# Performance work log

Hardware: AMD Instinct MI355X
Metric: run time of the kernel (lower is better)

Reference implementation:

```python
import jax, jax.numpy as jnp
import numpy as np

N, P, VEC, M = 100000, 96, 4, 70000
GROUPS = [27, 8, 8]
K = sum(GROUPS)  # 43
# Replicates the original's use of the LOCAL per-group offset index i_k when
# selecting attention weights in the output accumulation loop.
ATTN_IDX = np.concatenate([np.arange(g) for g in GROUPS]).astype(np.int32)


def setup_inputs() -> dict:
    key = jax.random.key(0)
    ks = jax.random.split(key, 12)
    rng = np.random.default_rng(0)
    # Kernel maps: per offset, M (in_idx, out_idx) pairs; out indices unique per
    # offset (each output point has at most one neighbor at a given offset).
    kmaps = np.stack([
        np.stack([rng.integers(0, N, M), rng.permutation(N)[:M]], axis=1)
        for _ in range(K)
    ]).astype(np.int32)  # [K, M, 2]
    w = lambda k, shape: jax.random.normal(k, shape, jnp.float32) * 0.05
    return dict(
        x=w(ks[0], (N, P)),
        coords=jax.random.uniform(ks[1], (N, 3), jnp.float32, 0.0, 100.0),
        Wq1=w(ks[2], (27, P, P)), gq1=jnp.ones(P), bq1=jnp.zeros(P),
        Wq2=w(ks[3], (27, P, VEC)), gq2=jnp.ones(VEC), bq2=jnp.zeros(VEC),
        Wv=w(ks[4], (27, P, P)), gv=jnp.ones(P), bv=jnp.zeros(P),
        Wp1=w(ks[5], (3, P)), gp1=jnp.ones(P), bp1=jnp.zeros(P),
        Wp2=w(ks[6], (P, VEC)), gp2=jnp.ones(VEC), bp2=jnp.zeros(VEC),
        W1=w(ks[7], (VEC, P)), b1=jnp.zeros(P),
        W2=w(ks[8], (P, VEC)), b2=jnp.zeros(VEC),
        g_out=jnp.ones(P), b_out=jnp.zeros(P),
        kmaps=jnp.asarray(kmaps),
    )


def _bn(x, g, b, eps=1e-5):
    m = x.mean(0)
    v = x.var(0)
    return g * (x - m) * jax.lax.rsqrt(v + eps) + b


def _sparse_conv3(x, W, km27, n):
    # Minkowski kernel-size-3 sparse conv: out[dst] += x[src] @ W[k] per offset.
    def step(acc, kw):
        km, Wk = kw
        return acc.at[km[:, 1]].add(x[km[:, 0]] @ Wk), None
    out, _ = jax.lax.scan(step, jnp.zeros((n, W.shape[-1]), x.dtype), (km27, W))
    return out


def _cbr(x, W, g, b, km27, n):
    return jax.nn.relu(_bn(_sparse_conv3(x, W, km27, n), g, b))


def _forward(x, coords, Wq1, gq1, bq1, Wq2, gq2, bq2, Wv, gv, bv,
             Wp1, gp1, bp1, Wp2, gp2, bp2, W1, b1, W2, b2, g_out, b_out, kmaps):
    n, p = x.shape
    rep = p // VEC  # expand_vec_dim factor
    km27 = kmaps[:27]
    # q branch: two conv3-BN-ReLU stages -> [N, VEC]
    qf = _cbr(_cbr(x, Wq1, gq1, bq1, km27, n), Wq2, gq2, bq2, km27, n)
    # v branch: conv3-BN-ReLU -> [N, P]
    vf = _cbr(x, Wv, gv, bv, km27, n)
    # positional encoding: two 1x1 conv-BN-ReLU on coords -> [N, VEC] -> [N, P]
    pe = jax.nn.relu(_bn(jax.nn.relu(_bn(coords @ Wp1, gp1, bp1)) @ Wp2, gp2, bp2))
    v_f = vf + jnp.repeat(pe, rep, axis=1)

    def attn_step(carry, km):
        src, dst = km[:, 0], km[:, 1]
        # presence mask of offset-k neighbors (scatter of x features, zero elsewhere)
        sm = jnp.zeros((n, p), x.dtype).at[dst].set(x[src])
        mask = jax.lax.stop_gradient((jnp.abs(sm).sum(-1) > 0).astype(x.dtype))  # [N]
        gq = jnp.zeros((n, VEC), x.dtype).at[dst].set(qf[src])
        d = gq - qf * mask[:, None]
        logits = (jax.nn.relu(d @ W1 + b1) @ W2 + b2) * mask[:, None]
        return carry, (logits, mask)

    _, (logits, masks) = jax.lax.scan(attn_step, None, kmaps)  # [K,N,VEC], [K,N]
    attn = jax.nn.softmax(logits, axis=0)  # softmax across the K stacked offsets
    attn_sel = attn[jnp.asarray(ATTN_IDX)]  # replicate local-index selection bug

    def out_step(acc, inp):
        km, mask, a = inp
        nv = jnp.zeros((n, p), x.dtype).at[km[:, 1]].set(v_f[km[:, 0]]) * mask[:, None]
        return acc + nv * jnp.repeat(a, rep, axis=1), None

    out, _ = jax.lax.scan(out_step, jnp.zeros((n, p), x.dtype),
                          (kmaps, masks, attn_sel))
    # out BN + ReLU, residual (inplanes == planes so res = x)
    return jax.nn.relu(_bn(out, g_out, b_out)) + x


def reference(x, coords, Wq1, gq1, bq1, Wq2, gq2, bq2, Wv, gv, bv,
              Wp1, gp1, bp1, Wp2, gp2, bp2, W1, b1, W2, b2, g_out, b_out, kmaps):
    return _forward(x, coords, Wq1, gq1, bq1, Wq2, gq2, bq2, Wv, gv, bv,
                    Wp1, gp1, bp1, Wp2, gp2, bp2, W1, b1, W2, b2,
                    g_out, b_out, kmaps)
```

## Files before the change

### kernel.cpp

```cpp
#include <hip/hip_runtime.h>
#include <math.h>

#define N_  100000
#define P_  96
#define V_  4
#define M_  70000
#define K_  43
#define KC_ 27

typedef unsigned short u16;
typedef __attribute__((ext_vector_type(8))) short bf16x8;
typedef __attribute__((ext_vector_type(4))) float f32x4;
typedef __attribute__((ext_vector_type(16))) float f32x16;

__device__ __forceinline__ u16 f2bf(float f) {
    unsigned int u = __float_as_uint(f);
    u += 0x7fffu + ((u >> 16) & 1u);
    return (u16)(u >> 16);
}
__device__ __forceinline__ float bf2f(u16 h) {
    return __uint_as_float(((unsigned int)h) << 16);
}

__device__ __forceinline__ void gl_lds16(const u16* g, u16* l) {
    __builtin_amdgcn_global_load_lds(
        (const __attribute__((address_space(1))) void*)g,
        (__attribute__((address_space(3))) void*)l, 16, 0, 0);
}

__global__ __launch_bounds__(256) void k_build_srcof(const int* __restrict__ km,
                                                     int* __restrict__ srcOf) {
    int idx = blockIdx.x * 256 + threadIdx.x;
    if (idx >= K_ * M_) return;
    int k = idx / M_;
    int e = idx - k * M_;
    const int* p = km + (size_t)(k * M_ + e) * 2;
    srcOf[(size_t)k * N_ + p[1]] = p[0];
}

__global__ __launch_bounds__(256) void k_rowabs_cvt(const float* __restrict__ x,
                                                    float* __restrict__ rowAbs,
                                                    u16* __restrict__ xb) {
    int row = blockIdx.x * 4 + (threadIdx.x >> 6);
    int lane = threadIdx.x & 63;
    if (row >= N_) return;
    const float* xr = x + (size_t)row * 96;
    float s = 0.f;
    for (int j = lane; j < 96; j += 64) {
        float v = xr[j];
        s += fabsf(v);
        xb[(size_t)row * 96 + j] = f2bf(v);
    }
#pragma unroll
    for (int o = 32; o > 0; o >>= 1) s += __shfl_down(s, o, 64);
    if (lane == 0) rowAbs[row] = s;
}

__global__ __launch_bounds__(256) void k_wt96p(const float* __restrict__ W,
                                               u16* __restrict__ Wp) {
    int idx = blockIdx.x * 256 + threadIdx.x;
    if (idx >= KC_ * 96 * 96) return;
    int k = idx / 9216, rem = idx - k * 9216, n = rem / 96, j = rem - n * 96;
    Wp[(size_t)k * 10240 + n * 104 + j] = f2bf(W[(size_t)k * 9216 + j * 96 + n]);
}

__global__ __launch_bounds__(256) void k_wt4(const float* __restrict__ W,
                                             u16* __restrict__ Wt) {
    int idx = blockIdx.x * 256 + threadIdx.x;
    if (idx >= KC_ * 16 * 96) return;
    int k = idx / 1536, rem = idx - k * 1536, n = rem / 96, j = rem - n * 96;
    Wt[idx] = (n < 4) ? f2bf(W[(size_t)k * 384 + j * 4 + n]) : (u16)0;
}

__global__ __launch_bounds__(256) void k_w12b(const float* __restrict__ W1,
                                              const float* __restrict__ W2,
                                              u16* __restrict__ w1b,
                                              u16* __restrict__ w2b) {
    int t = blockIdx.x * 256 + threadIdx.x;
    if (t < 96 * 32) {
        int j = t >> 5, c = t & 31;
        w1b[t] = (c < 4) ? f2bf(W1[c * 96 + j]) : (u16)0;
    }
    if (t < 16 * 96) {
        int n = t / 96, j = t - n * 96;
        w2b[t] = (n < 4) ? f2bf(W2[j * 4 + n]) : (u16)0;
    }
}

__global__ __launch_bounds__(384, 3) void k_conv96_dual(
    const u16* __restrict__ xb, const u16* __restrict__ Wqp,
    const u16* __restrict__ Wvp, const int* __restrict__ srcOf,
    u16* __restrict__ yQ, u16* __restrict__ yV,
    float* __restrict__ statsQ, float* __restrict__ statsV) {
    __shared__ u16 sA[192 * 104];
    __shared__ u16 sBq[10240];
    __shared__ u16 sBv[10240];
    const int r0 = blockIdx.x * 192;
    const int t = threadIdx.x;
    const int wv = t / 64, lane = t & 63;
    const int n32 = lane & 31, half = lane >> 5;
    const int ea = t >> 1, jca = (t & 1) * 6;
    f32x16 accq[3], accv[3];
#pragma unroll
    for (int i = 0; i < 3; i++) {
#pragma unroll
        for (int j = 0; j < 16; j++) { accq[i][j] = 0.f; accv[i][j] = 0.f; }
    }

    for (int k = 0; k < KC_; k++) {
        __syncthreads();
        {
            const u16* gq = Wqp + (size_t)k * 10240;
            const u16* gv = Wvp + (size_t)k * 10240;
            for (int i = wv; i < 40; i += 6) {
                int mv = (i >= 20);
                int off = (mv ? i - 20 : i) * 512 + lane * 8;
                gl_lds16((mv ? gv : gq) + off, (mv ? (u16*)sBv : (u16*)sBq) + off);
            }
        }
        {
            int r = r0 + ea;
            int src = (r < N_) ? srcOf[(size_t)k * N_ + r] : -1;
            if (src >= 0) {
                const uint4* sp = (const uint4*)(xb + (size_t)src * 96);
#pragma unroll
                for (int i = 0; i < 6; i++)
                    *(uint4*)(sA + ea * 104 + (jca + i) * 8) = sp[jca + i];
            } else {
                uint4 z = make_uint4(0, 0, 0, 0);
#pragma unroll
                for (int i = 0; i < 6; i++)
                    *(uint4*)(sA + ea * 104 + (jca + i) * 8) = z;
            }
        }
        __syncthreads();
#pragma unroll
        for (int ks = 0; ks < 6; ks++) {
            bf16x8 af = *(const bf16x8*)(sA + (wv * 32 + n32) * 104 + ks * 16 + half * 8);
#pragma unroll
            for (int nt = 0; nt < 3; nt++) {
                bf16x8 bq = *(const bf16x8*)(sBq + (nt * 32 + n32) * 104 + ks * 16 + half * 8);
                accq[nt] = __builtin_amdgcn_mfma_f32_32x32x16_bf16(af, bq, accq[nt], 0, 0, 0);
                bf16x8 bv = *(const bf16x8*)(sBv + (nt * 32 + n32) * 104 + ks * 16 + half * 8);
                accv[nt] = __builtin_amdgcn_mfma_f32_32x32x16_bf16(af, bv, accv[nt], 0, 0, 0);
            }
        }
    }
#pragma unroll
    for (int nt = 0; nt < 3; nt++) {
#pragma unroll
        for (int reg = 0; reg < 16; reg++) {
            int row = (reg & 3) + 8 * (reg >> 2) + 4 * half;
            int r = r0 + wv * 32 + row;
            if (r < N_) {
                yQ[(size_t)r * 96 + nt * 32 + n32] = f2bf(accq[nt][reg]);
                yV[(size_t)r * 96 + nt * 32 + n32] = f2bf(accv[nt][reg]);
            }
        }
    }
    __syncthreads();
    float* sred = (float*)sA;
    for (int pass = 0; pass < 2; pass++) {
        f32x16* acc = pass ? accv : accq;
        float* st = pass ? statsV : statsQ;
#pragma unroll
        for (int nt = 0; nt < 3; nt++) {
            float sv = 0.f, qv = 0.f;
#pragma unroll
            for (int reg = 0; reg < 16; reg++) {
                float a = acc[nt][reg];
                sv += a; qv += a * a;
            }
            sv += __shfl_xor(sv, 32, 64);
            qv += __shfl_xor(qv, 32, 64);
            if (half == 0) {
                sred[wv * 192 + nt * 32 + n32] = sv;
                sred[wv * 192 + 96 + nt * 32 + n32] = qv;
            }
        }
        __syncthreads();
        if (t < 192) {
            float tot = 0.f;
#pragma unroll
            for (int w = 0; w < 6; w++) tot += sred[w * 192 + t];
            atomicAdd(&st[t], tot);
        }
        __syncthreads();
    }
}

__global__ __launch_bounds__(256) void k_conv4_mfma(
    const u16* __restrict__ xbA, const u16* __restrict__ Wt4,
    const int* __restrict__ srcOf, float* __restrict__ qf) {
    __shared__ u16 sA[128 * 104];
    __shared__ u16 sB[16 * 104];
    const int r0 = blockIdx.x * 128;
    const int t = threadIdx.x;
    const int wv = t >> 6, lane = t & 63;
    const int m = lane & 15, quad = lane >> 4;
    const int ea = t >> 1, jca = (t & 1) * 6;
    f32x4 acc[2];
    acc[0] = (f32x4){0.f, 0.f, 0.f, 0.f};
    acc[1] = (f32x4){0.f, 0.f, 0.f, 0.f};
    for (int k = 0; k < KC_; k++) {
        __syncthreads();
        {
            int r = r0 + ea;
            int src = (r < N_) ? srcOf[(size_t)k * N_ + r] : -1;
            if (src >= 0) {
                const uint4* sp = (const uint4*)(xbA + (size_t)src * 96);
#pragma unroll
                for (int i = 0; i < 6; i++)
                    *(uint4*)(sA + ea * 104 + (jca + i) * 8) = sp[jca + i];
            } else {
                uint4 z = make_uint4(0, 0, 0, 0);
#pragma unroll
                for (int i = 0; i < 6; i++)
                    *(uint4*)(sA + ea * 104 + (jca + i) * 8) = z;
            }
        }
        if (t < 192) {
            int n = t / 12, jc = t - (t / 12) * 12;
            *(uint4*)(sB + n * 104 + jc * 8) =
                *(const uint4*)(Wt4 + (size_t)k * 1536 + n * 96 + jc * 8);
        }
        __syncthreads();
#pragma unroll
        for (int kk = 0; kk < 3; kk++) {
            bf16x8 bfr = *(const bf16x8*)(sB + m * 104 + kk * 32 + quad * 8);
#pragma unroll
            for (int rt = 0; rt < 2; rt++) {
                bf16x8 af = *(const bf16x8*)(sA + ((wv * 2 + rt) * 16 + m) * 104 + kk * 32 + quad * 8);
                acc[rt] = __builtin_amdgcn_mfma_f32_16x16x32_bf16(af, bfr, acc[rt], 0, 0, 0);
            }
        }
    }
    if (m < 4) {
#pragma unroll
        for (int rt = 0; rt < 2; rt++)
#pragma unroll
            for (int rg = 0; rg < 4; rg++) {
                int r = r0 + (wv * 2 + rt) * 16 + quad * 4 + rg;
                if (r < N_) qf[(size_t)r * 4 + m] = acc[rt][rg];
            }
    }
}

__global__ __launch_bounds__(192) void k_bnstats96(const float* __restrict__ xin,
                                                   float* __restrict__ stats) {
    __shared__ float sS[192], sQ[192];
    int t = threadIdx.x;
    int ch = t % 96, half = t / 96;
    float s = 0.f, q = 0.f;
    for (int r = blockIdx.x * 2 + half; r < N_; r += gridDim.x * 2) {
        float v = xin[(size_t)r * 96 + ch];
        s += v; q += v * v;
    }
    sS[t] = s; sQ[t] = q;
    __syncthreads();
    if (t < 96) {
        atomicAdd(&stats[ch], sS[t] + sS[t + 96]);
        atomicAdd(&stats[96 + ch], sQ[t] + sQ[t + 96]);
    }
}

__global__ __launch_bounds__(256) void k_bnstats4(const float* __restrict__ xin,
                                                  float* __restrict__ stats) {
    __shared__ float sS[256], sQ[256];
    int t = threadIdx.x;
    int c = t & 3, sub = t >> 2;
    float s = 0.f, q = 0.f;
    for (int r = blockIdx.x * 64 + sub; r < N_; r += gridDim.x * 64) {
        float v = xin[(size_t)r * 4 + c];
        s += v; q += v * v;
    }
    sS[t] = s; sQ[t] = q;
    __syncthreads();
    for (int off = 128; off >= 4; off >>= 1) {
        if (t < off) { sS[t] += sS[t + off]; sQ[t] += sQ[t + off]; }
        __syncthreads();
    }
    if (t < 4) {
        atomicAdd(&stats[t], sS[t]);
        atomicAdd(&stats[96 + t], sQ[t]);
    }
}

template <int C, int MODE>
__global__ __launch_bounds__(256) void k_bnapply(float* __restrict__ y,
                                                 const float* __restrict__ stats,
                                                 const float* __restrict__ g,
                                                 const float* __restrict__ b,
                                                 const float* __restrict__ aux) {
    int idx = blockIdx.x * 256 + threadIdx.x;
    if (idx >= N_ * C) return;
    int ch = idx % C;
    float mean = stats[ch] * (1.f / N_);
    float var = stats[96 + ch] * (1.f / N_) - mean * mean;
    float scale = g[ch] * rsqrtf(fmaxf(var, 0.f) + 1e-5f);
    float v = (y[idx] - mean) * scale + b[ch];
    v = fmaxf(v, 0.f);
    if (MODE == 2) v += aux[idx];
    y[idx] = v;
}

template <int MODE>
__global__ __launch_bounds__(256) void k_bnapply96_b2b(
    const u16* __restrict__ yin, const float* __restrict__ stats,
    const float* __restrict__ g, const float* __restrict__ b,
    const float* __restrict__ aux, u16* __restrict__ yout) {
    int idx = blockIdx.x * 256 + threadIdx.x;
    if (idx >= N_ * 96) return;
    int ch = idx % 96;
    float mean = stats[ch] * (1.f / N_);
    float var = stats[96 + ch] * (1.f / N_) - mean * mean;
    float scale = g[ch] * rsqrtf(fmaxf(var, 0.f) + 1e-5f);
    float v = (bf2f(yin[idx]) - mean) * scale + b[ch];
    v = fmaxf(v, 0.f);
    if (MODE == 1) { int r = idx / 96; v += aux[(size_t)r * 4 + (ch / 24)]; }
    yout[idx] = f2bf(v);
}

__global__ __launch_bounds__(256) void k_pe1(const float* __restrict__ coords,
                                             const float* __restrict__ Wp1,
                                             float* __restrict__ out) {
    int idx = blockIdx.x * 256 + threadIdx.x;
    if (idx >= N_ * 96) return;
    int r = idx / 96, ch = idx - r * 96;
    float c0 = coords[r * 3], c1 = coords[r * 3 + 1], c2 = coords[r * 3 + 2];
    out[idx] = c0 * Wp1[ch] + c1 * Wp1[96 + ch] + c2 * Wp1[192 + ch];
}

__global__ __launch_bounds__(256) void k_pe2(const float* __restrict__ hin,
                                             const float* __restrict__ Wp2,
                                             float* __restrict__ out) {
    int idx = blockIdx.x * 256 + threadIdx.x;
    if (idx >= N_ * 4) return;
    int r = idx / 4, c = idx & 3;
    const float* hr = hin + (size_t)r * 96;
    float acc = 0.f;
#pragma unroll 4
    for (int j = 0; j < 96; j++) acc += hr[j] * Wp2[j * 4 + c];
    out[idx] = acc;
}

__global__ __launch_bounds__(256) void k_attn_logits_mfma(
    const float* __restrict__ qf, const int* __restrict__ srcOf,
    const float* __restrict__ rowAbs,
    const u16* __restrict__ w1b, const float* __restrict__ b1,
    const u16* __restrict__ w2b, const float* __restrict__ b2,
    u16* __restrict__ wb) {
    __shared__ u16 hbuf[4][16 * 104];
    __shared__ u16 slogb[32][176];
    __shared__ u16 smk16[32][44];
    const int t = threadIdx.x;
    const int wv = t >> 6, lane = t & 63;
    const int col = lane & 15, quad = lane >> 4;
    const int r0 = blockIdx.x * 32;

    bf16x8 w1f[6];
    float b1v[6];
#pragma unroll
    for (int nt = 0; nt < 6; nt++) {
        w1f[nt] = *(const bf16x8*)(w1b + (nt * 16 + col) * 32 + quad * 8);
        b1v[nt] = b1[nt * 16 + col];
    }
    bf16x8 w2f[3];
#pragma unroll
    for (int kk = 0; kk < 3; kk++)
        w2f[kk] = *(const bf16x8*)(w2b + col * 96 + kk * 32 + quad * 8);
    float b2v = b2[col & 3];

    u16* hb = hbuf[wv];
    for (int tt = 0; tt < 22; tt++) {
        int tileBase = (wv * 22 + tt) * 16;
        bf16x8 af = (bf16x8){0, 0, 0, 0, 0, 0, 0, 0};
        if (quad == 0) {
            int P = tileBase + col;
            int rL = P / 44, k = P - rL * 44;
            int kc = (k < 43) ? k : 42;
            int r = r0 + rL;
            int s = srcOf[(size_t)kc * N_ + r];
            if (k == 43) s = -1;
            int sc = (s >= 0) ? s : 0;
            float mk = (s >= 0 && rowAbs[sc] > 0.f) ? 1.f : 0.f;
            float4 qs = *(const float4*)(qf + (size_t)sc * 4);
            float4 qr = *(const float4*)(qf + (size_t)r * 4);
            af[0] = (short)f2bf((qs.x - qr.x) * mk);
            af[1] = (short)f2bf((qs.y - qr.y) * mk);
            af[2] = (short)f2bf((qs.z - qr.z) * mk);
            af[3] = (short)f2bf((qs.w - qr.w) * mk);
            if (k < 43) smk16[rL][k] = (u16)(mk > 0.f ? 1 : 0);
        }
        f32x4 c1[6];
#pragma unroll
        for (int nt = 0; nt < 6; nt++) {
            c1[nt] = (f32x4){0.f, 0.f, 0.f, 0.f};
            c1[nt] = __builtin_amdgcn_mfma_f32_16x16x32_bf16(af, w1f[nt], c1[nt], 0, 0, 0);
        }
#pragma unroll
        for (int nt = 0; nt < 6; nt++) {
#pragma unroll
            for (int rg = 0; rg < 4; rg++) {
                float h = fmaxf(c1[nt][rg] + b1v[nt], 0.f);
                hb[(quad * 4 + rg) * 104 + nt * 16 + col] = f2bf(h);
            }
        }
        f32x4 acc2 = (f32x4){0.f, 0.f, 0.f, 0.f};
#pragma unroll
        for (int kk = 0; kk < 3; kk++) {
            bf16x8 a2 = *(const bf16x8*)(hb + col * 104 + kk * 32 + quad * 8);
            acc2 = __builtin_amdgcn_mfma_f32_16x16x32_bf16(a2, w2f[kk], acc2, 0, 0, 0);
        }
        if (col < 4) {
#pragma unroll
            for (int rg = 0; rg < 4; rg++) {
                int P = tileBase + quad * 4 + rg;
                int rL = P / 44, k = P - rL * 44;
                if (k < 43) {
                    float mval = (float)smk16[rL][k];
                    slogb[rL][k * 4 + col] = f2bf((acc2[rg] + b2v) * mval);
                }
            }
        }
    }
    __syncthreads();

    if (t < 128) {
        int rL = t >> 2, c = t & 3;
        float mx = 0.f;
        for (int k = 0; k < K_; k++) mx = fmaxf(mx, bf2f(slogb[rL][k * 4 + c]));
        float den = 0.f;
        for (int k = 0; k < K_; k++) den += __expf(bf2f(slogb[rL][k * 4 + c]) - mx);
        float inv = 1.f / den;
        for (int k = 0; k < K_; k++)
            slogb[rL][k * 4 + c] = f2bf(__expf(bf2f(slogb[rL][k * 4 + c]) - mx) * inv);
    }
    __syncthreads();

    for (int p = t; p < 32 * 43; p += 256) {
        int rL = p / 43, k = p - rL * 43;
        int idxk = (k < 27) ? k : ((k < 35) ? (k - 27) : (k - 35));
        u16 mk = smk16[rL][k];
        ushort4 wout = make_ushort4(0, 0, 0, 0);
        if (mk) {
            wout.x = slogb[rL][idxk * 4 + 0];
            wout.y = slogb[rL][idxk * 4 + 1];
            wout.z = slogb[rL][idxk * 4 + 2];
            wout.w = slogb[rL][idxk * 4 + 3];
        }
        *(ushort4*)(wb + ((size_t)(r0 + rL) * 44 + k) * 4) = wout;
    }
}

__global__ __launch_bounds__(256) void k_attn_gather(
    const u16* __restrict__ vfb, const u16* __restrict__ wb,
    const int* __restrict__ srcOf, float* __restrict__ out) {
    int idx = blockIdx.x * 256 + threadIdx.x;
    int r = idx / 24, c4 = idx - r * 24;
    if (r >= N_) return;
    int cg = c4 / 6;
    const u16* wrow = wb + (size_t)r * 176 + cg;
    float a0 = 0.f, a1 = 0.f, a2 = 0.f, a3 = 0.f;
    for (int k = 0; k < K_; k++) {
        int s = srcOf[(size_t)k * N_ + r];
        float w = bf2f(wrow[(size_t)k * 4]);
        w = (s >= 0) ? w : 0.f;
        int sc = (s >= 0) ? s : 0;
        ushort4 v = *(const ushort4*)(vfb + (size_t)sc * 96 + c4 * 4);
        a0 += w * bf2f(v.x);
        a1 += w * bf2f(v.y);
        a2 += w * bf2f(v.z);
        a3 += w * bf2f(v.w);
    }
    *(float4*)(out + (size_t)r * 96 + c4 * 4) = make_float4(a0, a1, a2, a3);
}

extern "C" void kernel_launch(void* const* d_in, const int* in_sizes, int n_in,
                              void* d_out, int out_size, void* d_ws, size_t ws_size,
                              hipStream_t stream) {
    const float* x      = (const float*)d_in[0];
    const float* coords = (const float*)d_in[1];
    const float* Wq1 = (const float*)d_in[2];
    const float* gq1 = (const float*)d_in[3];
    const float* bq1 = (const float*)d_in[4];
    const float* Wq2 = (const float*)d_in[5];
    const float* gq2 = (const float*)d_in[6];
    const float* bq2 = (const float*)d_in[7];
    const float* Wv  = (const float*)d_in[8];
    const float* gv  = (const float*)d_in[9];
    const float* bv  = (const float*)d_in[10];
    const float* Wp1 = (const float*)d_in[11];
    const float* gp1 = (const float*)d_in[12];
    const float* bp1 = (const float*)d_in[13];
    const float* Wp2 = (const float*)d_in[14];
    const float* gp2 = (const float*)d_in[15];
    const float* bp2 = (const float*)d_in[16];
    const float* W1  = (const float*)d_in[17];
    const float* b1  = (const float*)d_in[18];
    const float* W2  = (const float*)d_in[19];
    const float* b2  = (const float*)d_in[20];
    const float* g_out = (const float*)d_in[21];
    const float* b_out = (const float*)d_in[22];
    const int* kmaps = (const int*)d_in[23];
    float* out = (float*)d_out;

    char* ws = (char*)d_ws;
    int*   srcOf  = (int*)ws;
    float* rowAbs = (float*)(ws + 17200000);
    u16*   xb     = (u16*)(ws + 17600000);
    u16*   bufQb  = (u16*)(ws + 36800000);
    u16*   bufVb  = (u16*)(ws + 56000000);
    u16*   bufAb  = (u16*)(ws + 75200000);
    u16*   vfb    = (u16*)(ws + 75200000);
    float* pescr  = (float*)(ws + 17600000);
    u16*   wbuf   = (u16*)(ws + 17600000);
    float* qf     = (float*)(ws + 94400000);
    float* peb    = (float*)(ws + 96000000);
    u16*   Wq1p   = (u16*)(ws + 97600000);
    u16*   Wvp    = (u16*)(ws + 98152960);
    u16*   Wq2t   = (u16*)(ws + 98705920);
    u16*   w1b    = (u16*)(ws + 98788864);
    u16*   w2b    = (u16*)(ws + 98795008);
    float* stats  = (float*)(ws + 98798080);

    hipMemsetAsync(srcOf, 0xFF, (size_t)K_ * N_ * 4, stream);
    hipMemsetAsync(stats, 0, 6 * 192 * 4, stream);

    k_build_srcof<<<(K_ * M_ + 255) / 256, 256, 0, stream>>>(kmaps, srcOf);
    k_rowabs_cvt<<<N_ / 4, 256, 0, stream>>>(x, rowAbs, xb);
    k_wt96p<<<(KC_ * 9216 + 255) / 256, 256, 0, stream>>>(Wq1, Wq1p);
    k_wt96p<<<(KC_ * 9216 + 255) / 256, 256, 0, stream>>>(Wv, Wvp);
    k_wt4<<<(KC_ * 1536 + 255) / 256, 256, 0, stream>>>(Wq2, Wq2t);
    k_w12b<<<12, 256, 0, stream>>>(W1, W2, w1b, w2b);

    const int cbD  = (N_ + 191) / 192;
    const int cb4  = (N_ + 127) / 128;
    const int eb96 = N_ * 96 / 256;
    const int eb4  = (N_ * 4 + 255) / 256;

    k_conv96_dual<<<cbD, 384, 0, stream>>>(xb, Wq1p, Wvp, srcOf, bufQb, bufVb,
                                           stats + 0 * 192, stats + 4 * 192);

    k_bnapply96_b2b<0><<<eb96, 256, 0, stream>>>(bufQb, stats + 0 * 192, gq1, bq1, nullptr, bufAb);
    k_conv4_mfma<<<cb4, 256, 0, stream>>>(bufAb, Wq2t, srcOf, qf);
    k_bnstats4<<<512, 256, 0, stream>>>(qf, stats + 1 * 192);
    k_bnapply<4, 0><<<eb4, 256, 0, stream>>>(qf, stats + 1 * 192, gq2, bq2, nullptr);

    k_pe1<<<eb96, 256, 0, stream>>>(coords, Wp1, pescr);
    k_bnstats96<<<512, 192, 0, stream>>>(pescr, stats + 2 * 192);
    k_bnapply<96, 0><<<eb96, 256, 0, stream>>>(pescr, stats + 2 * 192, gp1, bp1, nullptr);
    k_pe2<<<eb4, 256, 0, stream>>>(pescr, Wp2, peb);
    k_bnstats4<<<512, 256, 0, stream>>>(peb, stats + 3 * 192);
    k_bnapply<4, 0><<<eb4, 256, 0, stream>>>(peb, stats + 3 * 192, gp2, bp2, nullptr);

    k_bnapply96_b2b<1><<<eb96, 256, 0, stream>>>(bufVb, stats + 4 * 192, gv, bv, peb, vfb);

    k_attn_logits_mfma<<<N_ / 32, 256, 0, stream>>>(qf, srcOf, rowAbs, w1b, b1, w2b, b2, wbuf);
    k_attn_gather<<<(N_ * 24) / 256, 256, 0, stream>>>(vfb, wbuf, srcOf, out);

    k_bnstats96<<<512, 192, 0, stream>>>(out, stats + 5 * 192);
    k_bnapply<96, 2><<<eb96, 256, 0, stream>>>(out, stats + 5 * 192, g_out, b_out, x);
}
```

Before: 1.003 ms.

## Pad gathered bf16 rows to 128 stride and coalesce conv gather loads

Stores the bf16 input activations and the first BN output with a 128-element row stride (256 bytes) instead of 96. The gather loops in the two sparse conv kernels are rebuilt so 12 of every 16 lanes each fetch one 16-byte chunk of a row, with 8 rows in flight per thread before writing to LDS. The aim is more memory-level parallelism and better-aligned, more coalesced row gathers. In exchange it uses more workspace and memory traffic for the padding, idles a quarter of the threads during the gather, and requires re-laid-out workspace offsets.

```diff
diff --git a/kernel.cpp b/kernel.cpp
--- a/kernel.cpp
+++ b/kernel.cpp
@@ -49,7 +49,7 @@
     for (int j = lane; j < 96; j += 64) {
         float v = xr[j];
         s += fabsf(v);
-        xb[(size_t)row * 96 + j] = f2bf(v);
+        xb[(size_t)row * 128 + j] = f2bf(v);
     }
 #pragma unroll
     for (int o = 32; o > 0; o >>= 1) s += __shfl_down(s, o, 64);
@@ -99,7 +99,8 @@
     const int t = threadIdx.x;
     const int wv = t / 64, lane = t & 63;
     const int n32 = lane & 31, half = lane >> 5;
-    const int ea = t >> 1, jca = (t & 1) * 6;
+    const int gc = t & 15;
+    const int grb = t >> 4;
     f32x16 accq[3], accv[3];
 #pragma unroll
     for (int i = 0; i < 3; i++) {
@@ -118,20 +119,20 @@
                 gl_lds16((mv ? gv : gq) + off, (mv ? (u16*)sBv : (u16*)sBq) + off);
             }
         }
-        {
-            int r = r0 + ea;
-            int src = (r < N_) ? srcOf[(size_t)k * N_ + r] : -1;
-            if (src >= 0) {
-                const uint4* sp = (const uint4*)(xb + (size_t)src * 96);
-#pragma unroll
-                for (int i = 0; i < 6; i++)
-                    *(uint4*)(sA + ea * 104 + (jca + i) * 8) = sp[jca + i];
-            } else {
-                uint4 z = make_uint4(0, 0, 0, 0);
-#pragma unroll
-                for (int i = 0; i < 6; i++)
-                    *(uint4*)(sA + ea * 104 + (jca + i) * 8) = z;
-            }
+        if (gc < 12) {
+            uint4 va[8];
+#pragma unroll
+            for (int j = 0; j < 8; j++) {
+                int rL = j * 24 + grb;
+                int r = r0 + rL;
+                int src = (r < N_) ? srcOf[(size_t)k * N_ + r] : -1;
+                va[j] = make_uint4(0, 0, 0, 0);
+                if (src >= 0)
+                    va[j] = *(const uint4*)(xb + (size_t)src * 128 + gc * 8);
+            }
+#pragma unroll
+            for (int j = 0; j < 8; j++)
+                *(uint4*)(sA + (j * 24 + grb) * 104 + gc * 8) = va[j];
         }
         __syncthreads();
 #pragma unroll
@@ -198,26 +199,27 @@
     const int t = threadIdx.x;
     const int wv = t >> 6, lane = t & 63;
     const int m = lane & 15, quad = lane >> 4;
-    const int ea = t >> 1, jca = (t & 1) * 6;
+    const int gc = t & 15;
+    const int grb = t >> 4;
     f32x4 acc[2];
     acc[0] = (f32x4){0.f, 0.f, 0.f, 0.f};
     acc[1] = (f32x4){0.f, 0.f, 0.f, 0.f};
     for (int k = 0; k < KC_; k++) {
         __syncthreads();
-        {
-            int r = r0 + ea;
-            int src = (r < N_) ? srcOf[(size_t)k * N_ + r] : -1;
-            if (src >= 0) {
-                const uint4* sp = (const uint4*)(xbA + (size_t)src * 96);
-#pragma unroll
-                for (int i = 0; i < 6; i++)
-                    *(uint4*)(sA + ea * 104 + (jca + i) * 8) = sp[jca + i];
-            } else {
-                uint4 z = make_uint4(0, 0, 0, 0);
-#pragma unroll
-                for (int i = 0; i < 6; i++)
-                    *(uint4*)(sA + ea * 104 + (jca + i) * 8) = z;
-            }
+        if (gc < 12) {
+            uint4 va[8];
+#pragma unroll
+            for (int j = 0; j < 8; j++) {
+                int rL = j * 16 + grb;
+                int r = r0 + rL;
+                int src = (r < N_) ? srcOf[(size_t)k * N_ + r] : -1;
+                va[j] = make_uint4(0, 0, 0, 0);
+                if (src >= 0)
+                    va[j] = *(const uint4*)(xbA + (size_t)src * 128 + gc * 8);
+            }
+#pragma unroll
+            for (int j = 0; j < 8; j++)
+                *(uint4*)(sA + (j * 16 + grb) * 104 + gc * 8) = va[j];
         }
         if (t < 192) {
             int n = t / 12, jc = t - (t / 12) * 12;
@@ -304,7 +306,7 @@
     y[idx] = v;
 }
 
-template <int MODE>
+template <int MODE, int OS>
 __global__ __launch_bounds__(256) void k_bnapply96_b2b(
     const u16* __restrict__ yin, const float* __restrict__ stats,
     const float* __restrict__ g, const float* __restrict__ b,
@@ -312,13 +314,14 @@
     int idx = blockIdx.x * 256 + threadIdx.x;
     if (idx >= N_ * 96) return;
     int ch = idx % 96;
+    int r = idx / 96;
     float mean = stats[ch] * (1.f / N_);
     float var = stats[96 + ch] * (1.f / N_) - mean * mean;
     float scale = g[ch] * rsqrtf(fmaxf(var, 0.f) + 1e-5f);
     float v = (bf2f(yin[idx]) - mean) * scale + b[ch];
     v = fmaxf(v, 0.f);
-    if (MODE == 1) { int r = idx / 96; v += aux[(size_t)r * 4 + (ch / 24)]; }
-    yout[idx] = f2bf(v);
+    if (MODE == 1) v += aux[(size_t)r * 4 + (ch / 24)];
+    yout[(size_t)r * OS + ch] = f2bf(v);
 }
 
 __global__ __launch_bounds__(256) void k_pe1(const float* __restrict__ coords,
@@ -508,21 +511,21 @@
     char* ws = (char*)d_ws;
     int*   srcOf  = (int*)ws;
     float* rowAbs = (float*)(ws + 17200000);
-    u16*   xb     = (u16*)(ws + 17600000);
-    u16*   bufQb  = (u16*)(ws + 36800000);
-    u16*   bufVb  = (u16*)(ws + 56000000);
-    u16*   bufAb  = (u16*)(ws + 75200000);
-    u16*   vfb    = (u16*)(ws + 75200000);
-    float* pescr  = (float*)(ws + 17600000);
-    u16*   wbuf   = (u16*)(ws + 17600000);
-    float* qf     = (float*)(ws + 94400000);
-    float* peb    = (float*)(ws + 96000000);
-    u16*   Wq1p   = (u16*)(ws + 97600000);
-    u16*   Wvp    = (u16*)(ws + 98152960);
-    u16*   Wq2t   = (u16*)(ws + 98705920);
-    u16*   w1b    = (u16*)(ws + 98788864);
-    u16*   w2b    = (u16*)(ws + 98795008);
-    float* stats  = (float*)(ws + 98798080);
+    float* stats  = (float*)(ws + 17600000);
+    u16*   Wq1p   = (u16*)(ws + 17604608);
+    u16*   Wvp    = (u16*)(ws + 18157568);
+    u16*   Wq2t   = (u16*)(ws + 18710528);
+    u16*   w1b    = (u16*)(ws + 18793472);
+    u16*   w2b    = (u16*)(ws + 18799616);
+    u16*   xb     = (u16*)(ws + 18802688);
+    u16*   bufQb  = (u16*)(ws + 44402688);
+    u16*   bufVb  = (u16*)(ws + 63602688);
+    u16*   bufAb  = (u16*)(ws + 18802688);
+    float* pescr  = (float*)(ws + 18802688);
+    u16*   vfb    = (u16*)(ws + 18802688);
+    u16*   wbuf   = (u16*)(ws + 38002688);
+    float* qf     = (float*)(ws + 82802688);
+    float* peb    = (float*)(ws + 84402688);
 
     hipMemsetAsync(srcOf, 0xFF, (size_t)K_ * N_ * 4, stream);
     hipMemsetAsync(stats, 0, 6 * 192 * 4, stream);
@@ -542,7 +545,7 @@
     k_conv96_dual<<<cbD, 384, 0, stream>>>(xb, Wq1p, Wvp, srcOf, bufQb, bufVb,
                                            stats + 0 * 192, stats + 4 * 192);
 
-    k_bnapply96_b2b<0><<<eb96, 256, 0, stream>>>(bufQb, stats + 0 * 192, gq1, bq1, nullptr, bufAb);
+    k_bnapply96_b2b<0, 128><<<eb96, 256, 0, stream>>>(bufQb, stats + 0 * 192, gq1, bq1, nullptr, bufAb);
     k_conv4_mfma<<<cb4, 256, 0, stream>>>(bufAb, Wq2t, srcOf, qf);
     k_bnstats4<<<512, 256, 0, stream>>>(qf, stats + 1 * 192);
     k_bnapply<4, 0><<<eb4, 256, 0, stream>>>(qf, stats + 1 * 192, gq2, bq2, nullptr);
@@ -554,7 +557,7 @@
     k_bnstats4<<<512, 256, 0, stream>>>(peb, stats + 3 * 192);
     k_bnapply<4, 0><<<eb4, 256, 0, stream>>>(peb, stats + 3 * 192, gp2, bp2, nullptr);
 
-    k_bnapply96_b2b<1><<<eb96, 256, 0, stream>>>(bufVb, stats + 4 * 192, gv, bv, peb, vfb);
+    k_bnapply96_b2b<1, 96><<<eb96, 256, 0, stream>>>(bufVb, stats + 4 * 192, gv, bv, peb, vfb);
 
     k_attn_logits_mfma<<<N_ / 32, 256, 0, stream>>>(qf, srcOf, rowAbs, w1b, b1, w2b, b2, wbuf);
     k_attn_gather<<<(N_ * 24) / 256, 256, 0, stream>>>(vfb, wbuf, srcOf, out);
```

After: 1.182 ms. +17.9%, slower.

## Prefetch next offset's gathered rows into registers during MFMA compute

Applied to the files above, without the earlier changes.

Both sparse-conv kernels now gather the source rows for the next kernel offset into registers (plus a two-ahead source index) while the current offset's MFMAs run. The rows are then written to LDS after the next barrier. This hides global gather latency behind matrix compute. The cost is 24 extra VGPRs per thread in a kernel already launched with bounds for 3 blocks per CU, which risks spills or lower occupancy. The barrier at the loop top now waits only on lgkmcnt, so the outstanding register gathers are not waited on before it.

```diff
diff --git a/kernel.cpp b/kernel.cpp
--- a/kernel.cpp
+++ b/kernel.cpp
@@ -100,6 +100,8 @@
     const int wv = t / 64, lane = t & 63;
     const int n32 = lane & 31, half = lane >> 5;
     const int ea = t >> 1, jca = (t & 1) * 6;
+    const int r = r0 + ea;
+    const bool rv = (r < N_);
     f32x16 accq[3], accv[3];
 #pragma unroll
     for (int i = 0; i < 3; i++) {
@@ -107,8 +109,24 @@
         for (int j = 0; j < 16; j++) { accq[i][j] = 0.f; accv[i][j] = 0.f; }
     }
 
+    uint4 va[6];
+    int sNext;
+    {
+        int s0 = rv ? srcOf[r] : -1;
+#pragma unroll
+        for (int i = 0; i < 6; i++) va[i] = make_uint4(0, 0, 0, 0);
+        if (s0 >= 0) {
+            const uint4* sp = (const uint4*)(xb + (size_t)s0 * 96);
+#pragma unroll
+            for (int i = 0; i < 6; i++) va[i] = sp[jca + i];
+        }
+        sNext = rv ? srcOf[(size_t)N_ + r] : -1;
+    }
+
     for (int k = 0; k < KC_; k++) {
-        __syncthreads();
+        asm volatile("s_waitcnt lgkmcnt(0)" ::: "memory");
+        __builtin_amdgcn_s_barrier();
+        __builtin_amdgcn_sched_barrier(0);
         {
             const u16* gq = Wqp + (size_t)k * 10240;
             const u16* gv = Wvp + (size_t)k * 10240;
@@ -118,22 +136,22 @@
                 gl_lds16((mv ? gv : gq) + off, (mv ? (u16*)sBv : (u16*)sBq) + off);
             }
         }
-        {
-            int r = r0 + ea;
-            int src = (r < N_) ? srcOf[(size_t)k * N_ + r] : -1;
-            if (src >= 0) {
-                const uint4* sp = (const uint4*)(xb + (size_t)src * 96);
-#pragma unroll
-                for (int i = 0; i < 6; i++)
-                    *(uint4*)(sA + ea * 104 + (jca + i) * 8) = sp[jca + i];
-            } else {
-                uint4 z = make_uint4(0, 0, 0, 0);
-#pragma unroll
-                for (int i = 0; i < 6; i++)
-                    *(uint4*)(sA + ea * 104 + (jca + i) * 8) = z;
-            }
-        }
+#pragma unroll
+        for (int i = 0; i < 6; i++)
+            *(uint4*)(sA + ea * 104 + (jca + i) * 8) = va[i];
         __syncthreads();
+        int sCur = sNext;
+        if (k + 1 < KC_) {
+            sNext = rv ? srcOf[(size_t)(k + 2) * N_ + r] : -1;
+#pragma unroll
+            for (int i = 0; i < 6; i++) va[i] = make_uint4(0, 0, 0, 0);
+            if (sCur >= 0) {
+                const uint4* sp = (const uint4*)(xb + (size_t)sCur * 96);
+#pragma unroll
+                for (int i = 0; i < 6; i++) va[i] = sp[jca + i];
+            }
+        }
+        __builtin_amdgcn_sched_barrier(0);
 #pragma unroll
         for (int ks = 0; ks < 6; ks++) {
             bf16x8 af = *(const bf16x8*)(sA + (wv * 32 + n32) * 104 + ks * 16 + half * 8);
@@ -151,10 +169,10 @@
 #pragma unroll
         for (int reg = 0; reg < 16; reg++) {
             int row = (reg & 3) + 8 * (reg >> 2) + 4 * half;
-            int r = r0 + wv * 32 + row;
-            if (r < N_) {
-                yQ[(size_t)r * 96 + nt * 32 + n32] = f2bf(accq[nt][reg]);
-                yV[(size_t)r * 96 + nt * 32 + n32] = f2bf(accv[nt][reg]);
+            int rr = r0 + wv * 32 + row;
+            if (rr < N_) {
+                yQ[(size_t)rr * 96 + nt * 32 + n32] = f2bf(accq[nt][reg]);
+                yV[(size_t)rr * 96 + nt * 32 + n32] = f2bf(accv[nt][reg]);
             }
         }
     }
@@ -199,32 +217,51 @@
     const int wv = t >> 6, lane = t & 63;
     const int m = lane & 15, quad = lane >> 4;
     const int ea = t >> 1, jca = (t & 1) * 6;
+    const int r = r0 + ea;
+    const bool rv = (r < N_);
     f32x4 acc[2];
     acc[0] = (f32x4){0.f, 0.f, 0.f, 0.f};
     acc[1] = (f32x4){0.f, 0.f, 0.f, 0.f};
+
+    uint4 va[6];
+    int sNext;
+    {
+        int s0 = rv ? srcOf[r] : -1;
+#pragma unroll
+        for (int i = 0; i < 6; i++) va[i] = make_uint4(0, 0, 0, 0);
+        if (s0 >= 0) {
+            const uint4* sp = (const uint4*)(xbA + (size_t)s0 * 96);
+#pragma unroll
+            for (int i = 0; i < 6; i++) va[i] = sp[jca + i];
+        }
+        sNext = rv ? srcOf[(size_t)N_ + r] : -1;
+    }
+
     for (int k = 0; k < KC_; k++) {
-        __syncthreads();
-        {
-            int r = r0 + ea;
-            int src = (r < N_) ? srcOf[(size_t)k * N_ + r] : -1;
-            if (src >= 0) {
-                const uint4* sp = (const uint4*)(xbA + (size_t)src * 96);
-#pragma unroll
-                for (int i = 0; i < 6; i++)
-                    *(uint4*)(sA + ea * 104 + (jca + i) * 8) = sp[jca + i];
-            } else {
-                uint4 z = make_uint4(0, 0, 0, 0);
-#pragma unroll
-                for (int i = 0; i < 6; i++)
-                    *(uint4*)(sA + ea * 104 + (jca + i) * 8) = z;
-            }
-        }
+        asm volatile("s_waitcnt lgkmcnt(0)" ::: "memory");
+        __builtin_amdgcn_s_barrier();
+        __builtin_amdgcn_sched_barrier(0);
         if (t < 192) {
             int n = t / 12, jc = t - (t / 12) * 12;
             *(uint4*)(sB + n * 104 + jc * 8) =
                 *(const uint4*)(Wt4 + (size_t)k * 1536 + n * 96 + jc * 8);
         }
+#pragma unroll
+        for (int i = 0; i < 6; i++)
+            *(uint4*)(sA + ea * 104 + (jca + i) * 8) = va[i];
         __syncthreads();
+        int sCur = sNext;
+        if (k + 1 < KC_) {
+            sNext = rv ? srcOf[(size_t)(k + 2) * N_ + r] : -1;
+#pragma unroll
+            for (int i = 0; i < 6; i++) va[i] = make_uint4(0, 0, 0, 0);
+            if (sCur >= 0) {
+                const uint4* sp = (const uint4*)(xbA + (size_t)sCur * 96);
+#pragma unroll
+                for (int i = 0; i < 6; i++) va[i] = sp[jca + i];
+            }
+        }
+        __builtin_amdgcn_sched_barrier(0);
 #pragma unroll
         for (int kk = 0; kk < 3; kk++) {
             bf16x8 bfr = *(const bf16x8*)(sB + m * 104 + kk * 32 + quad * 8);
@@ -240,8 +277,8 @@
         for (int rt = 0; rt < 2; rt++)
 #pragma unroll
             for (int rg = 0; rg < 4; rg++) {
-                int r = r0 + (wv * 2 + rt) * 16 + quad * 4 + rg;
-                if (r < N_) qf[(size_t)r * 4 + m] = acc[rt][rg];
+                int rr = r0 + (wv * 2 + rt) * 16 + quad * 4 + rg;
+                if (rr < N_) qf[(size_t)rr * 4 + m] = acc[rt][rg];
             }
     }
 }
```

New measurement: 1.014 ms. Within noise of the previous version (+1.1%).

## Software-pipeline sparse conv gathers into registers with double-buffered weight LDS

Applied to the files above, without the earlier changes.

Both gather-convolution kernels stop staging gathered activation rows through shared memory. Instead each lane loads its MFMA A-fragment straight from global into registers, and the next offset's fragment is prefetched one step ahead. Source indices are prefetched two steps ahead. In the dual 96-channel conv, weights are double-buffered in LDS with async global-to-LDS copies and a partial vmcnt wait, which removes one barrier per offset. A zeroed row in the output buffer stands in for missing neighbors so the gather path has no branch. This costs extra registers and issues more scattered global loads per lane.

```diff
diff --git a/kernel.cpp b/kernel.cpp
--- a/kernel.cpp
+++ b/kernel.cpp
@@ -90,16 +90,17 @@
 __global__ __launch_bounds__(384, 3) void k_conv96_dual(
     const u16* __restrict__ xb, const u16* __restrict__ Wqp,
     const u16* __restrict__ Wvp, const int* __restrict__ srcOf,
+    const u16* __restrict__ zrow,
     u16* __restrict__ yQ, u16* __restrict__ yV,
     float* __restrict__ statsQ, float* __restrict__ statsV) {
-    __shared__ u16 sA[192 * 104];
-    __shared__ u16 sBq[10240];
-    __shared__ u16 sBv[10240];
+    __shared__ u16 sBB[2 * 2 * 10240];
     const int r0 = blockIdx.x * 192;
     const int t = threadIdx.x;
     const int wv = t / 64, lane = t & 63;
     const int n32 = lane & 31, half = lane >> 5;
-    const int ea = t >> 1, jca = (t & 1) * 6;
+    const int row = r0 + wv * 32 + n32;
+    const bool rv = (row < N_);
+    const int rowS = rv ? row : 0;
     f32x16 accq[3], accv[3];
 #pragma unroll
     for (int i = 0; i < 3; i++) {
@@ -107,59 +108,85 @@
         for (int j = 0; j < 16; j++) { accq[i][j] = 0.f; accv[i][j] = 0.f; }
     }
 
-    for (int k = 0; k < KC_; k++) {
-        __syncthreads();
-        {
-            const u16* gq = Wqp + (size_t)k * 10240;
-            const u16* gv = Wvp + (size_t)k * 10240;
-            for (int i = wv; i < 40; i += 6) {
-                int mv = (i >= 20);
-                int off = (mv ? i - 20 : i) * 512 + lane * 8;
-                gl_lds16((mv ? gv : gq) + off, (mv ? (u16*)sBv : (u16*)sBq) + off);
-            }
-        }
-        {
-            int r = r0 + ea;
-            int src = (r < N_) ? srcOf[(size_t)k * N_ + r] : -1;
-            if (src >= 0) {
-                const uint4* sp = (const uint4*)(xb + (size_t)src * 96);
-#pragma unroll
-                for (int i = 0; i < 6; i++)
-                    *(uint4*)(sA + ea * 104 + (jca + i) * 8) = sp[jca + i];
-            } else {
-                uint4 z = make_uint4(0, 0, 0, 0);
-#pragma unroll
-                for (int i = 0; i < 6; i++)
-                    *(uint4*)(sA + ea * 104 + (jca + i) * 8) = z;
-            }
-        }
-        __syncthreads();
+    bf16x8 va0[6], va1[6];
+    int sPre;
+    {
+        int s0 = srcOf[rowS];
+        const u16* xp = (rv && s0 >= 0) ? (xb + (size_t)s0 * 96 + half * 8)
+                                        : (zrow + half * 8);
+        __builtin_amdgcn_sched_barrier(0);
+#pragma unroll
+        for (int j = 0; j < 7; j++) {
+            int i = wv * 7 + j; if (i >= 40) i -= 2;
+            int mv = (i >= 20) ? 1 : 0;
+            int off = (i - 20 * mv) * 512 + lane * 8;
+            gl_lds16((mv ? Wvp : Wqp) + off, (u16*)sBB + mv * 10240 + off);
+        }
+        __builtin_amdgcn_sched_barrier(0);
+#pragma unroll
+        for (int i = 0; i < 6; i++) va0[i] = *(const bf16x8*)(xp + i * 16);
+        sPre = srcOf[(size_t)N_ + rowS];
+    }
+
+    auto STEP = [&](int k, int bufR, bf16x8 (&vaC)[6], bf16x8 (&vaN)[6]) {
+        asm volatile("s_waitcnt vmcnt(7)" ::: "memory");
+        __builtin_amdgcn_s_barrier();
+        __builtin_amdgcn_sched_barrier(0);
+        const u16* sbR = (const u16*)sBB + bufR * 20480;
+        if (k + 1 < KC_) {
+            int s = sPre;
+            const u16* xpN = (rv && s >= 0) ? (xb + (size_t)s * 96 + half * 8)
+                                            : (zrow + half * 8);
+            __builtin_amdgcn_sched_barrier(0);
+            u16* sbW = (u16*)sBB + (1 - bufR) * 20480;
+            const u16* gq = Wqp + (size_t)(k + 1) * 10240;
+            const u16* gv = Wvp + (size_t)(k + 1) * 10240;
+#pragma unroll
+            for (int j = 0; j < 7; j++) {
+                int i = wv * 7 + j; if (i >= 40) i -= 2;
+                int mv = (i >= 20) ? 1 : 0;
+                int off = (i - 20 * mv) * 512 + lane * 8;
+                gl_lds16((mv ? gv : gq) + off, sbW + mv * 10240 + off);
+            }
+            __builtin_amdgcn_sched_barrier(0);
+#pragma unroll
+            for (int i = 0; i < 6; i++) vaN[i] = *(const bf16x8*)(xpN + i * 16);
+            int k2 = (k + 2 < KC_) ? (k + 2) : 0;
+            sPre = srcOf[(size_t)k2 * N_ + rowS];
+        }
+        __builtin_amdgcn_sched_barrier(0);
 #pragma unroll
         for (int ks = 0; ks < 6; ks++) {
-            bf16x8 af = *(const bf16x8*)(sA + (wv * 32 + n32) * 104 + ks * 16 + half * 8);
+            bf16x8 af = vaC[ks];
 #pragma unroll
             for (int nt = 0; nt < 3; nt++) {
-                bf16x8 bq = *(const bf16x8*)(sBq + (nt * 32 + n32) * 104 + ks * 16 + half * 8);
+                bf16x8 bq = *(const bf16x8*)(sbR + (nt * 32 + n32) * 104 + ks * 16 + half * 8);
                 accq[nt] = __builtin_amdgcn_mfma_f32_32x32x16_bf16(af, bq, accq[nt], 0, 0, 0);
-                bf16x8 bv = *(const bf16x8*)(sBv + (nt * 32 + n32) * 104 + ks * 16 + half * 8);
+                bf16x8 bv = *(const bf16x8*)(sbR + 10240 + (nt * 32 + n32) * 104 + ks * 16 + half * 8);
                 accv[nt] = __builtin_amdgcn_mfma_f32_32x32x16_bf16(af, bv, accv[nt], 0, 0, 0);
             }
         }
-    }
+    };
+    for (int kp = 0; kp < 26; kp += 2) {
+        STEP(kp, 0, va0, va1);
+        STEP(kp + 1, 1, va1, va0);
+    }
+    STEP(26, 0, va0, va1);
+
 #pragma unroll
     for (int nt = 0; nt < 3; nt++) {
 #pragma unroll
         for (int reg = 0; reg < 16; reg++) {
-            int row = (reg & 3) + 8 * (reg >> 2) + 4 * half;
-            int r = r0 + wv * 32 + row;
-            if (r < N_) {
-                yQ[(size_t)r * 96 + nt * 32 + n32] = f2bf(accq[nt][reg]);
-                yV[(size_t)r * 96 + nt * 32 + n32] = f2bf(accv[nt][reg]);
+            int rr0 = (reg & 3) + 8 * (reg >> 2) + 4 * half;
+            int rr = r0 + wv * 32 + rr0;
+            if (rr < N_) {
+                yQ[(size_t)rr * 96 + nt * 32 + n32] = f2bf(accq[nt][reg]);
+                yV[(size_t)rr * 96 + nt * 32 + n32] = f2bf(accv[nt][reg]);
             }
         }
     }
     __syncthreads();
-    float* sred = (float*)sA;
+    float* sred = (float*)sBB;
     for (int pass = 0; pass < 2; pass++) {
         f32x16* acc = pass ? accv : accq;
         float* st = pass ? statsV : statsQ;
@@ -189,60 +216,76 @@
     }
 }
 
-__global__ __launch_bounds__(256) void k_conv4_mfma(
+__global__ __launch_bounds__(256, 4) void k_conv4_mfma(
     const u16* __restrict__ xbA, const u16* __restrict__ Wt4,
-    const int* __restrict__ srcOf, float* __restrict__ qf) {
-    __shared__ u16 sA[128 * 104];
-    __shared__ u16 sB[16 * 104];
+    const int* __restrict__ srcOf, const u16* __restrict__ zrow,
+    float* __restrict__ qf) {
     const int r0 = blockIdx.x * 128;
     const int t = threadIdx.x;
     const int wv = t >> 6, lane = t & 63;
     const int m = lane & 15, quad = lane >> 4;
-    const int ea = t >> 1, jca = (t & 1) * 6;
-    f32x4 acc[2];
-    acc[0] = (f32x4){0.f, 0.f, 0.f, 0.f};
-    acc[1] = (f32x4){0.f, 0.f, 0.f, 0.f};
-    for (int k = 0; k < KC_; k++) {
-        __syncthreads();
-        {
-            int r = r0 + ea;
-            int src = (r < N_) ? srcOf[(size_t)k * N_ + r] : -1;
-            if (src >= 0) {
-                const uint4* sp = (const uint4*)(xbA + (size_t)src * 96);
-#pragma unroll
-                for (int i = 0; i < 6; i++)
-                    *(uint4*)(sA + ea * 104 + (jca + i) * 8) = sp[jca + i];
-            } else {
-                uint4 z = make_uint4(0, 0, 0, 0);
-#pragma unroll
-                for (int i = 0; i < 6; i++)
-                    *(uint4*)(sA + ea * 104 + (jca + i) * 8) = z;
-            }
-        }
-        if (t < 192) {
-            int n = t / 12, jc = t - (t / 12) * 12;
-            *(uint4*)(sB + n * 104 + jc * 8) =
-                *(const uint4*)(Wt4 + (size_t)k * 1536 + n * 96 + jc * 8);
-        }
-        __syncthreads();
+    const int rowA = r0 + wv * 32 + m;
+    const int rowB = rowA + 16;
+    const bool rvA = rowA < N_, rvB = rowB < N_;
+    const int rsA = rvA ? rowA : 0, rsB = rvB ? rowB : 0;
+    f32x4 acc0 = (f32x4){0.f, 0.f, 0.f, 0.f};
+    f32x4 acc1 = (f32x4){0.f, 0.f, 0.f, 0.f};
+    bf16x8 a0[2][3], a1[2][3], b0[3], b1[3];
+    int sPA, sPB;
+    {
+        int sa = srcOf[rsA], sb = srcOf[rsB];
+        const u16* xpA = (rvA && sa >= 0) ? (xbA + (size_t)sa * 96 + quad * 8)
+                                          : (zrow + quad * 8);
+        const u16* xpB = (rvB && sb >= 0) ? (xbA + (size_t)sb * 96 + quad * 8)
+                                          : (zrow + quad * 8);
+        const u16* wp = Wt4 + m * 96 + quad * 8;
 #pragma unroll
         for (int kk = 0; kk < 3; kk++) {
-            bf16x8 bfr = *(const bf16x8*)(sB + m * 104 + kk * 32 + quad * 8);
-#pragma unroll
-            for (int rt = 0; rt < 2; rt++) {
-                bf16x8 af = *(const bf16x8*)(sA + ((wv * 2 + rt) * 16 + m) * 104 + kk * 32 + quad * 8);
-                acc[rt] = __builtin_amdgcn_mfma_f32_16x16x32_bf16(af, bfr, acc[rt], 0, 0, 0);
-            }
-        }
-    }
+            a0[0][kk] = *(const bf16x8*)(xpA + kk * 32);
+            a0[1][kk] = *(const bf16x8*)(xpB + kk * 32);
+            b0[kk]    = *(const bf16x8*)(wp + kk * 32);
+        }
+        sPA = srcOf[(size_t)N_ + rsA];
+        sPB = srcOf[(size_t)N_ + rsB];
+    }
+    auto STEP = [&](int k, bf16x8 (&aC)[2][3], bf16x8 (&bC)[3],
+                    bf16x8 (&aN)[2][3], bf16x8 (&bN)[3]) {
+        if (k + 1 < KC_) {
+            int sa = sPA, sb = sPB;
+            const u16* xpA = (rvA && sa >= 0) ? (xbA + (size_t)sa * 96 + quad * 8)
+                                              : (zrow + quad * 8);
+            const u16* xpB = (rvB && sb >= 0) ? (xbA + (size_t)sb * 96 + quad * 8)
+                                              : (zrow + quad * 8);
+            const u16* wp = Wt4 + (size_t)(k + 1) * 1536 + m * 96 + quad * 8;
+#pragma unroll
+            for (int kk = 0; kk < 3; kk++) {
+                aN[0][kk] = *(const bf16x8*)(xpA + kk * 32);
+                aN[1][kk] = *(const bf16x8*)(xpB + kk * 32);
+                bN[kk]    = *(const bf16x8*)(wp + kk * 32);
+            }
+            int k2 = (k + 2 < KC_) ? (k + 2) : 0;
+            sPA = srcOf[(size_t)k2 * N_ + rsA];
+            sPB = srcOf[(size_t)k2 * N_ + rsB];
+        }
+#pragma unroll
+        for (int kk = 0; kk < 3; kk++) {
+            acc0 = __builtin_amdgcn_mfma_f32_16x16x32_bf16(aC[0][kk], bC[kk], acc0, 0, 0, 0);
+            acc1 = __builtin_amdgcn_mfma_f32_16x16x32_bf16(aC[1][kk], bC[kk], acc1, 0, 0, 0);
+        }
+    };
+    for (int kp = 0; kp < 26; kp += 2) {
+        STEP(kp, a0, b0, a1, b1);
+        STEP(kp + 1, a1, b1, a0, b0);
+    }
+    STEP(26, a0, b0, a1, b1);
     if (m < 4) {
 #pragma unroll
-        for (int rt = 0; rt < 2; rt++)
-#pragma unroll
-            for (int rg = 0; rg < 4; rg++) {
-                int r = r0 + (wv * 2 + rt) * 16 + quad * 4 + rg;
-                if (r < N_) qf[(size_t)r * 4 + m] = acc[rt][rg];
-            }
+        for (int rg = 0; rg < 4; rg++) {
+            int rA = r0 + wv * 32 + quad * 4 + rg;
+            if (rA < N_) qf[(size_t)rA * 4 + m] = acc0[rg];
+            int rB = rA + 16;
+            if (rB < N_) qf[(size_t)rB * 4 + m] = acc1[rg];
+        }
     }
 }
 
@@ -524,8 +567,11 @@
     u16*   w2b    = (u16*)(ws + 98795008);
     float* stats  = (float*)(ws + 98798080);
 
+    const u16* zrow = (const u16*)out;
+
     hipMemsetAsync(srcOf, 0xFF, (size_t)K_ * N_ * 4, stream);
     hipMemsetAsync(stats, 0, 6 * 192 * 4, stream);
+    hipMemsetAsync(out, 0, 192, stream);
 
     k_build_srcof<<<(K_ * M_ + 255) / 256, 256, 0, stream>>>(kmaps, srcOf);
     k_rowabs_cvt<<<N_ / 4, 256, 0, stream>>>(x, rowAbs, xb);
@@ -539,11 +585,11 @@
     const int eb96 = N_ * 96 / 256;
     const int eb4  = (N_ * 4 + 255) / 256;
 
-    k_conv96_dual<<<cbD, 384, 0, stream>>>(xb, Wq1p, Wvp, srcOf, bufQb, bufVb,
+    k_conv96_dual<<<cbD, 384, 0, stream>>>(xb, Wq1p, Wvp, srcOf, zrow, bufQb, bufVb,
                                            stats + 0 * 192, stats + 4 * 192);
 
     k_bnapply96_b2b<0><<<eb96, 256, 0, stream>>>(bufQb, stats + 0 * 192, gq1, bq1, nullptr, bufAb);
-    k_conv4_mfma<<<cb4, 256, 0, stream>>>(bufAb, Wq2t, srcOf, qf);
+    k_conv4_mfma<<<cb4, 256, 0, stream>>>(bufAb, Wq2t, srcOf, zrow, qf);
     k_bnstats4<<<512, 256, 0, stream>>>(qf, stats + 1 * 192);
     k_bnapply<4, 0><<<eb4, 256, 0, stream>>>(qf, stats + 1 * 192, gq2, bq2, nullptr);
 
```

Result: slower. 1.065 ms (+6.2%).
